# Kernel tuning notes

Hardware: AMD Instinct MI355X
Metric: run time of the kernel (lower is better)

The kernel has to match this reference:

```python
import jax, jax.numpy as jnp
import numpy as np

B = 8192  # batch of 28x28 single-channel images
N_WIRES = 4
N_PATCH = 14 * 14  # 196 2x2 patches per image


def _apply_ry(state, wire, theta):
    """Apply RY(theta) on `wire` to a batched real statevector [N,2,2,2,2].
    RY = [[cos(t/2), -sin(t/2)], [sin(t/2), cos(t/2)]] is real, so the whole
    circuit (RY + CNOT) keeps amplitudes real."""
    half = theta * 0.5
    c, s = jnp.cos(half), jnp.sin(half)
    if jnp.ndim(c) > 0:  # per-patch data angle of shape [N]
        c = c[:, None, None, None]
        s = s[:, None, None, None]
    st = jnp.moveaxis(state, 1 + wire, -1)
    a0, a1 = st[..., 0], st[..., 1]
    st = jnp.stack([c * a0 - s * a1, s * a0 + c * a1], axis=-1)
    return jnp.moveaxis(st, -1, 1 + wire)


def _cnot(state, ctrl):
    """CNOT with control=ctrl, target=ctrl+1: flip target bit where control=1."""
    c0 = jnp.take(state, 0, axis=1 + ctrl)
    # after removing the control axis, the target axis (orig 2+ctrl) is at 1+ctrl
    c1 = jnp.flip(jnp.take(state, 1, axis=1 + ctrl), axis=1 + ctrl)
    return jnp.stack([c0, c1], axis=1 + ctrl)


def _circuit(angles, var_params):
    """Batched 4-qubit statevector sim. angles: [N,4] -> <Z_i>: [N,4]."""
    n = angles.shape[0]
    state = jnp.zeros((n, 2, 2, 2, 2), angles.dtype).at[:, 0, 0, 0, 0].set(1.0)
    for i in range(N_WIRES):
        state = _apply_ry(state, i, angles[:, i])
    for i in range(N_WIRES):
        state = _apply_ry(state, i, var_params[0, i])
    for i in range(N_WIRES - 1):
        state = _cnot(state, i)
    for i in range(N_WIRES):
        state = _apply_ry(state, i, var_params[1, i])
    p = state * state  # Born probabilities (real amplitudes)
    margs = [jnp.sum(p, axis=tuple(a for a in range(1, 5) if a != 1 + i)) for i in range(N_WIRES)]
    return jnp.stack([m[:, 0] - m[:, 1] for m in margs], axis=-1)  # [N,4]


def setup_inputs() -> dict:
    key = jax.random.key(0)
    k = jax.random.split(key, 6)
    return {
        "x": jax.random.uniform(k[0], (B, 1, 28, 28), dtype=jnp.float32),
        "var_params": jax.random.normal(k[1], (2, N_WIRES), dtype=jnp.float32),
        "map_w": jax.random.normal(k[2], (8, 4), dtype=jnp.float32),
        "map_b": jax.random.normal(k[3], (8,), dtype=jnp.float32),
        "lin_w": jax.random.normal(k[4], (10, N_PATCH * 8), dtype=jnp.float32),
        "lin_b": jax.random.normal(k[5], (10,), dtype=jnp.float32),
    }


def reference(x, var_params, map_w, map_b, lin_w, lin_b):
    bsz = x.shape[0]
    img = x.reshape(bsz, 28, 28)
    # extract 2x2 patches, row-major over (r, c), pixel order (dr*2+dc)
    patches = img.reshape(bsz, 14, 2, 14, 2).transpose(0, 1, 3, 2, 4).reshape(bsz * N_PATCH, 4)
    angles = patches / 255.0
    meas = _circuit(angles, var_params)            # [B*196, 4]
    feat = meas @ map_w.T + map_b                   # [B*196, 8]
    flat = feat.reshape(bsz, N_PATCH * 8)           # [B, 1568]
    logits = flat @ lin_w.T + lin_b                 # [B, 10]
    return jax.nn.log_softmax(logits, axis=-1)
```

## Files before the change

kernel.cpp:

```cpp
#include <hip/hip_runtime.h>


#define WS_M   32
#define NWAVES 2048

__global__ __launch_bounds__(256) void quanv_pre(
    const float* __restrict__ vp,
    const float* __restrict__ map_w,
    const float* __restrict__ map_b,
    const float* __restrict__ lin_w,
    const float* __restrict__ lin_b,
    float* __restrict__ ws)
{
    const int k = blockIdx.x;
    const int p = threadIdx.x;
    __shared__ float s_part[4];

    float pb = 0.0f;
    if (p < 196) {
        const float* lw = lin_w + k * 1568 + p * 8;
        const float4 w0 = *(const float4*)lw;
        const float4 w1 = *(const float4*)(lw + 4);
        const float l[8] = {w0.x, w0.y, w0.z, w0.w, w1.x, w1.y, w1.z, w1.w};
        float m[4] = {0.f, 0.f, 0.f, 0.f};
        #pragma unroll
        for (int j = 0; j < 8; ++j) {
            #pragma unroll
            for (int i = 0; i < 4; ++i)
                m[i] = fmaf(l[j], map_w[j * 4 + i], m[i]);
            pb = fmaf(l[j], map_b[j], pb);
        }
        #pragma unroll
        for (int i = 0; i < 4; ++i)
            ws[WS_M + (k * 4 + i) * 256 + p] = m[i];
    } else {
        #pragma unroll
        for (int i = 0; i < 4; ++i)
            ws[WS_M + (k * 4 + i) * 256 + p] = 0.0f;
    }

    #pragma unroll
    for (int off = 32; off; off >>= 1) pb += __shfl_xor(pb, off, 64);
    if ((p & 63) == 0) s_part[p >> 6] = pb;
    __syncthreads();
    if (p == 0)
        ws[16 + k] = lin_b[k] + s_part[0] + s_part[1] + s_part[2] + s_part[3];
    if (k == 0 && p < 4) {
        ws[p]      = cosf(vp[p]);
        ws[4 + p]  = sinf(vp[p]);
        ws[8 + p]  = cosf(vp[4 + p]);
        ws[12 + p] = sinf(vp[4 + p]);
    }
}

__global__ __launch_bounds__(256, 2) void quanv_main(
    const float* __restrict__ x,
    const float* __restrict__ ws,
    float* __restrict__ out, int B)
{
    const int lane = threadIdx.x & 63;
    const int wave = blockIdx.x * 4 + (threadIdx.x >> 6);
    if (wave >= B) return;

    float cva[4], sva[4], cth[4], sth[4];
    #pragma unroll
    for (int i = 0; i < 4; ++i) {
        cva[i] = ws[i];     sva[i] = ws[4 + i];
        cth[i] = ws[8 + i]; sth[i] = ws[12 + i];
    }
    float bias[10];
    #pragma unroll
    for (int k = 0; k < 10; ++k) bias[k] = ws[16 + k];

    float Mr[10][4][4];
    #pragma unroll
    for (int k = 0; k < 10; ++k)
        #pragma unroll
        for (int i = 0; i < 4; ++i)
            #pragma unroll
            for (int j = 0; j < 4; ++j)
                Mr[k][i][j] = ws[WS_M + (k * 4 + i) * 256 + j * 64 + lane];

    int off0[4], off1[4];
    #pragma unroll
    for (int j = 0; j < 4; ++j) {
        int p = j * 64 + lane;
        p = p > 195 ? 195 : p;
        const int py = p / 14;
        const int px = p - py * 14;
        off0[j] = py * 56 + px * 2;
        off1[j] = off0[j] + 28;
    }

    float2 nq0[4], nq1[4];
    {
        const float* img = x + (size_t)wave * 784;
        #pragma unroll
        for (int j = 0; j < 4; ++j) {
            nq0[j] = *(const float2*)(img + off0[j]);
            nq1[j] = *(const float2*)(img + off1[j]);
        }
    }

    for (int b = wave; b < B; b += NWAVES) {
        float2 q0[4], q1[4];
        #pragma unroll
        for (int j = 0; j < 4; ++j) { q0[j] = nq0[j]; q1[j] = nq1[j]; }

        int bn = b + NWAVES;
        bn = bn < B ? bn : b;
        {
            const float* img = x + (size_t)bn * 784;
            #pragma unroll
            for (int j = 0; j < 4; ++j) {
                nq0[j] = *(const float2*)(img + off0[j]);
                nq1[j] = *(const float2*)(img + off1[j]);
            }
        }

        float lg[10];
        #pragma unroll
        for (int k = 0; k < 10; ++k) lg[k] = 0.0f;

        #pragma unroll
        for (int j = 0; j < 4; ++j) {
            const float t[4] = {q0[j].x, q0[j].y, q1[j].x, q1[j].y};
            float C[4], S[4];
            #pragma unroll
            for (int i = 0; i < 4; ++i) {
                const float a  = t[i] * (1.0f / 255.0f);
                const float a2 = a * a;
                const float ct = fmaf(a2, -0.5f, 1.0f);
                const float st = a * fmaf(a2, -1.0f / 6.0f, 1.0f);
                C[i] = fmaf(cva[i], ct, -sva[i] * st);
                S[i] = fmaf(sva[i], ct,  cva[i] * st);
            }
            const float P1 = C[0] * C[1], P2 = P1 * C[2], P3 = P2 * C[3];
            const float m0 = fmaf(cth[0], C[0], -sth[0] * (S[0] * S[1]));
            const float m1 = fmaf(cth[1], P1,   -sth[1] * (S[1] * S[2]));
            const float m2 = fmaf(cth[2], P2,   -sth[2] * (S[2] * S[3]));
            const float m3 = fmaf(cth[3], P3,   -sth[3] * S[3]);
            #pragma unroll
            for (int k = 0; k < 10; ++k)
                lg[k] = fmaf(m0, Mr[k][0][j],
                        fmaf(m1, Mr[k][1][j],
                        fmaf(m2, Mr[k][2][j],
                        fmaf(m3, Mr[k][3][j], lg[k]))));
        }

        #pragma unroll
        for (int k = 0; k < 10; ++k) {
            float v = lg[k];
            #pragma unroll
            for (int off = 32; off; off >>= 1) v += __shfl_xor(v, off, 64);
            lg[k] = v;
        }

        if (lane == 0) {
            float logits[10], mx = -1e30f;
            #pragma unroll
            for (int k = 0; k < 10; ++k) {
                logits[k] = lg[k] + bias[k];
                mx = fmaxf(mx, logits[k]);
            }
            float sum = 0.0f;
            #pragma unroll
            for (int k = 0; k < 10; ++k) sum += __expf(logits[k] - mx);
            const float lse = mx + __logf(sum);
            float* o = out + (size_t)b * 10;
            #pragma unroll
            for (int k = 0; k < 10; k += 2)
                *(float2*)(o + k) = make_float2(logits[k] - lse,
                                                logits[k + 1] - lse);
        }
    }
}

extern "C" void kernel_launch(void* const* d_in, const int* in_sizes, int n_in,
                              void* d_out, int out_size, void* d_ws, size_t ws_size,
                              hipStream_t stream) {
    const float* x     = (const float*)d_in[0];
    const float* vp    = (const float*)d_in[1];
    const float* map_w = (const float*)d_in[2];
    const float* map_b = (const float*)d_in[3];
    const float* lin_w = (const float*)d_in[4];
    const float* lin_b = (const float*)d_in[5];
    float* out = (float*)d_out;
    float* ws  = (float*)d_ws;

    const int B = in_sizes[0] / 784;

    quanv_pre<<<10, 256, 0, stream>>>(vp, map_w, map_b, lin_w, lin_b, ws);
    quanv_main<<<NWAVES / 4, 256, 0, stream>>>(x, ws, out, B);
}
```

Measured before the change: 87.39 us.

## Pack folded weights to fp16 and use dot2 with DPP wave reduction

```diff
diff --git a/kernel.cpp b/kernel.cpp
--- a/kernel.cpp
+++ b/kernel.cpp
@@ -1,8 +1,49 @@
 #include <hip/hip_runtime.h>
 
-
-#define WS_M   32
-#define NWAVES 2048
+typedef _Float16 half2_t __attribute__((ext_vector_type(2)));
+
+
+#define WS_MOFF 32
+#define NWAVES  2048
+
+static __device__ __forceinline__ half2_t pk2(float a, float b) {
+#if __has_builtin(__builtin_amdgcn_cvt_pkrtz)
+    return __builtin_bit_cast(half2_t, __builtin_amdgcn_cvt_pkrtz(a, b));
+#else
+    half2_t r; r.x = (_Float16)a; r.y = (_Float16)b; return r;
+#endif
+}
+
+static __device__ __forceinline__ float fdot2f(half2_t a, half2_t b, float c) {
+#if __has_builtin(__builtin_amdgcn_fdot2)
+    return __builtin_amdgcn_fdot2(a, b, c, false);
+#else
+    return c + (float)a.x * (float)b.x + (float)a.y * (float)b.y;
+#endif
+}
+
+#if __has_builtin(__builtin_amdgcn_update_dpp)
+template <int CTRL>
+static __device__ __forceinline__ float dpp_add(float x) {
+    int t = __builtin_amdgcn_update_dpp(0, __float_as_int(x), CTRL, 0xf, 0xf, false);
+    return x + __int_as_float(t);
+}
+static __device__ __forceinline__ float wave_sum(float x) {
+    x = dpp_add<0x111>(x);
+    x = dpp_add<0x112>(x);
+    x = dpp_add<0x114>(x);
+    x = dpp_add<0x118>(x);
+    x = dpp_add<0x142>(x);
+    x = dpp_add<0x143>(x);
+    return x;
+}
+#else
+static __device__ __forceinline__ float wave_sum(float x) {
+    #pragma unroll
+    for (int off = 32; off; off >>= 1) x += __shfl_xor(x, off, 64);
+    return x;
+}
+#endif
 
 __global__ __launch_bounds__(256) void quanv_pre(
     const float* __restrict__ vp,
@@ -16,6 +57,8 @@
     const int p = threadIdx.x;
     __shared__ float s_part[4];
 
+    half2_t* Mws = (half2_t*)(ws + WS_MOFF);
+
     float pb = 0.0f;
     if (p < 196) {
         const float* lw = lin_w + k * 1568 + p * 8;
@@ -30,13 +73,9 @@
                 m[i] = fmaf(l[j], map_w[j * 4 + i], m[i]);
             pb = fmaf(l[j], map_b[j], pb);
         }
-        #pragma unroll
-        for (int i = 0; i < 4; ++i)
-            ws[WS_M + (k * 4 + i) * 256 + p] = m[i];
-    } else {
-        #pragma unroll
-        for (int i = 0; i < 4; ++i)
-            ws[WS_M + (k * 4 + i) * 256 + p] = 0.0f;
+        const float sc = (p >= 192) ? 0.0625f : 1.0f;
+        Mws[(k * 2 + 0) * 256 + p] = pk2(m[0] * sc, m[1] * sc);
+        Mws[(k * 2 + 1) * 256 + p] = pk2(m[2] * sc, m[3] * sc);
     }
 
     #pragma unroll
@@ -53,7 +92,7 @@
     }
 }
 
-__global__ __launch_bounds__(256, 2) void quanv_main(
+__global__ __launch_bounds__(256, 3) void quanv_main(
     const float* __restrict__ x,
     const float* __restrict__ ws,
     float* __restrict__ out, int B)
@@ -68,24 +107,26 @@
         cva[i] = ws[i];     sva[i] = ws[4 + i];
         cth[i] = ws[8 + i]; sth[i] = ws[12 + i];
     }
-    float bias[10];
-    #pragma unroll
-    for (int k = 0; k < 10; ++k) bias[k] = ws[16 + k];
-
-    float Mr[10][4][4];
+
+    int pidx[4];
+    #pragma unroll
+    for (int j = 0; j < 3; ++j) pidx[j] = j * 64 + lane;
+    pidx[3] = 192 + (lane & 3);
+
+    const half2_t* Mws = (const half2_t*)(ws + WS_MOFF);
+    half2_t Mr[10][2][4];
     #pragma unroll
     for (int k = 0; k < 10; ++k)
         #pragma unroll
-        for (int i = 0; i < 4; ++i)
+        for (int h = 0; h < 2; ++h)
             #pragma unroll
             for (int j = 0; j < 4; ++j)
-                Mr[k][i][j] = ws[WS_M + (k * 4 + i) * 256 + j * 64 + lane];
+                Mr[k][h][j] = Mws[(k * 2 + h) * 256 + pidx[j]];
 
     int off0[4], off1[4];
     #pragma unroll
     for (int j = 0; j < 4; ++j) {
-        int p = j * 64 + lane;
-        p = p > 195 ? 195 : p;
+        const int p  = pidx[j];
         const int py = p / 14;
         const int px = p - py * 14;
         off0[j] = py * 56 + px * 2;
@@ -140,27 +181,23 @@
             const float m1 = fmaf(cth[1], P1,   -sth[1] * (S[1] * S[2]));
             const float m2 = fmaf(cth[2], P2,   -sth[2] * (S[2] * S[3]));
             const float m3 = fmaf(cth[3], P3,   -sth[3] * S[3]);
+
+            const half2_t h01 = pk2(m0, m1);
+            const half2_t h23 = pk2(m2, m3);
             #pragma unroll
             for (int k = 0; k < 10; ++k)
-                lg[k] = fmaf(m0, Mr[k][0][j],
-                        fmaf(m1, Mr[k][1][j],
-                        fmaf(m2, Mr[k][2][j],
-                        fmaf(m3, Mr[k][3][j], lg[k]))));
-        }
-
-        #pragma unroll
-        for (int k = 0; k < 10; ++k) {
-            float v = lg[k];
-            #pragma unroll
-            for (int off = 32; off; off >>= 1) v += __shfl_xor(v, off, 64);
-            lg[k] = v;
-        }
-
-        if (lane == 0) {
+                lg[k] = fdot2f(h01, Mr[k][0][j],
+                         fdot2f(h23, Mr[k][1][j], lg[k]));
+        }
+
+        #pragma unroll
+        for (int k = 0; k < 10; ++k) lg[k] = wave_sum(lg[k]);
+
+        if (lane == 63) {
             float logits[10], mx = -1e30f;
             #pragma unroll
             for (int k = 0; k < 10; ++k) {
-                logits[k] = lg[k] + bias[k];
+                logits[k] = lg[k] + ws[16 + k];
                 mx = fmaxf(mx, logits[k]);
             }
             float sum = 0.0f;
```

Result: faster. 84.86 us (-2.9%).
